# Performance work log

Measured on AMD Instinct MI355X. Metric: run time of the kernel, lower is better.

Reference implementation:

```python
import jax, jax.numpy as jnp
import numpy as np

N, H, B, D, O = 512, 40, 8, 384, 62
DT = 1e-4  # step_size
BOUND = 500.0  # coupling saturation bound
# Jansen-Rit constants (ParamsJR defaults, all variances 0 -> non-learnable)
A_, a_, B_, b_, g_ = 3.25, 100.0, 22.0, 50.0, 100.0
c1, c2, c3, c4 = 135.0, 135.0 * 0.8, 135.0 * 0.25, 135.0 * 0.25
STD_IN, VMAX, V0, R_, MU, K_, KI = 100.0, 5.0, 6.0, 0.56, 0.5, 5.0, 1.0


def setup_inputs() -> dict:
    key = jax.random.key(0)
    ks = jax.random.split(key, 9)
    return {
        "input": jax.random.normal(ks[0], (N, H, B), jnp.float32),
        "noise_in": jax.random.normal(ks[1], (N, H, B, 1), jnp.float32),
        "noise_out": jax.random.normal(ks[2], (N, B), jnp.float32),
        "hx": jax.random.uniform(ks[3], (N, 6), jnp.float32),
        "hE": jax.random.normal(ks[4], (N, D), jnp.float32),
        "w_bb": jax.random.normal(ks[5], (N, N), jnp.float32),
        "sc": jax.random.uniform(ks[6], (N, N), jnp.float32),
        "lm": jax.random.normal(ks[7], (O, N), jnp.float32),
        "delays": jax.random.randint(ks[8], (N, N), 0, D, jnp.int32),
    }


def _sigmoid(x):
    # potential-to-rate operator
    return VMAX / (1.0 + jnp.exp(R_ * (V0 - x)))


def _sys2nd(Aamp, a, u, x, v):
    return Aamp * a * u - 2.0 * a * v - a * a * x


def reference(input, noise_in, noise_out, hx, hE, w_bb, sc, lm, delays):
    # normalized symmetric coupling matrix
    w = jnp.exp(w_bb) * sc
    ws = jnp.log1p(0.5 * (w + w.T))
    w_n = ws / jnp.linalg.norm(ws)            # Frobenius norm, as torch.linalg.norm
    rowsum = jnp.sum(w_n, axis=1)[:, None]    # dg = -diag(rowsum); dg @ x == -rowsum*x

    M, E, I = hx[:, 0:1], hx[:, 1:2], hx[:, 2:3]
    Mv, Ev, Iv = hx[:, 3:4], hx[:, 4:5], hx[:, 5:6]

    def hidden_step(carry, inp):
        M, E, I, Mv, Ev, Iv, hE = carry
        u, nz = inp  # [N,1] each
        Ed = jnp.take_along_axis(hE, delays, axis=1)      # Ed[i,j] = hE[i, delays[i,j]]
        LEd = jnp.sum(w_n * Ed.T, axis=1, keepdims=True)  # [N,1]
        noiseE = nz * STD_IN
        stim = K_ * KI * u
        rM = _sigmoid(E - I)
        rE = c2 * _sigmoid(c1 * M)
        rI = c4 * _sigmoid(c3 * M)
        coupled = g_ * (LEd - rowsum * (E - I))
        coupling = BOUND * jnp.tanh(coupled / BOUND)
        Mn = M + DT * Mv
        En = E + DT * Ev
        In = I + DT * Iv
        Mvn = Mv + DT * _sys2nd(A_, a_, rM, M, Mv)
        Evn = Ev + DT * _sys2nd(A_, a_, rE + coupling + stim + noiseE + MU, E, Ev)
        Ivn = Iv + DT * _sys2nd(B_, b_, rI, I, Iv)
        hE = hE.at[:, 0].set(En[:, 0] - In[:, 0])  # in-place slot-0 write, as in torch
        return (Mn, En, In, Mvn, Evn, Ivn, hE), None

    def batch_step(state, inp):
        u_seq, nz_seq = inp  # [H,N,1]
        state, _ = jax.lax.scan(hidden_step, state, (u_seq, nz_seq))
        M, E, I, Mv, Ev, Iv, hE = state
        hE = jnp.concatenate([E - I, hE[:, :-1]], axis=1)  # shift delay buffer
        eeg = 0.0005 * (lm @ (E - I))  # [O,1]
        return (M, E, I, Mv, Ev, Iv, hE), (M, E, I, Mv, Ev, Iv, eeg)

    u_all = jnp.transpose(input, (2, 1, 0))[..., None]            # [B,H,N,1]
    nz_all = jnp.transpose(noise_in[..., 0], (2, 1, 0))[..., None]
    state0 = (M, E, I, Mv, Ev, Iv, hE)
    state, outs = jax.lax.scan(batch_step, state0, (u_all, nz_all))
    Ms, Es, Is, Mvs, Evs, Ivs, eegs = outs  # [B,N,1] each, eeg [B,O,1]

    stack = lambda x: x[..., 0].T  # -> [N,B] (or [O,B]), matches torch.cat(axis=1)
    Mf, Ef, If, Mvf, Evf, Ivf, hEf = state
    current_state = jnp.concatenate([Mf, Ef, If, Mvf, Evf, Ivf], axis=1)  # [N,6]
    return (current_state, stack(eegs), stack(Es), stack(Is), stack(Ms),
            stack(Evs), stack(Ivs), stack(Mvs), hEf)
```

## Files before the change

### kernel.cpp

```cpp
#include <hip/hip_runtime.h>
#include <math.h>

#define N_    512
#define H_    40
#define B_N   8
#define D_    384
#define O_    62
#define RW    392
#define SMAX  13
#define CMAX  28

#define OUT_STATE 0
#define OUT_EEG   3072
#define OUT_ES    3568
#define OUT_IS    7664
#define OUT_MS    11760
#define OUT_EVS   15856
#define OUT_IVS   19952
#define OUT_MVS   24048
#define OUT_HE    28144

#define SIGK      0.8079092228978195f
#define SIGC      4.847455337386917f
#define SIGK_E    109.06774509120563f
#define SIGK_I    27.266936272801407f
#define TANHS     0.5770780163555854f

#define BARRIER() asm volatile("s_waitcnt lgkmcnt(0)\n\ts_barrier" ::: "memory")

__global__ void k_prep(const float* __restrict__ input, const float* __restrict__ noise_in,
                       float* __restrict__ drv,
                       const float* __restrict__ wbb, const float* __restrict__ sc,
                       const float* __restrict__ hE_in, const int* __restrict__ delays,
                       float* __restrict__ ws, float* __restrict__ ring,
                       float* __restrict__ rowsum_ws, float* __restrict__ sumsq,
                       float* __restrict__ s0w, int* __restrict__ s0j, int* __restrict__ s0c,
                       float* __restrict__ s1w, int* __restrict__ s1p) {
    int i = blockIdx.x;
    int t = threadIdx.x;
    __shared__ float wsrow[N_];
    __shared__ float red[256];
    __shared__ int cnt_c[8];
    __shared__ int bases[8];
    __shared__ int runbase;

    if (i < H_ * B_N) {
        int b = i & 7, h = i >> 3;
        int dst = (b * H_ + h) * N_;
        for (int n = t; n < N_; n += 256) {
            float u  = input[n * (H_ * B_N) + h * B_N + b];
            float nz = noise_in[n * (H_ * B_N) + h * B_N + b];
            drv[dst + n] = fmaf(0.1625f, u, fmaf(3.25f, nz, 16.26625f));
        }
    }

    if (t < SMAX) { s0j[t * N_ + i] = i;        s0w[t * N_ + i] = 0.f; }
    if (t < CMAX) { s1p[t * N_ + i] = (1 << 9); s1w[t * N_ + i] = 0.f; }
    if (t < 9)    { ring[i * RW + t] = 0.f; }

    float ssq = 0.f, rsum = 0.f;
    for (int j = t; j < N_; j += 256) {
        float w = 0.5f * (expf(wbb[i * N_ + j]) * sc[i * N_ + j] +
                          expf(wbb[j * N_ + i]) * sc[j * N_ + i]);
        float v = log1pf(w);
        ws[i * N_ + j] = v;
        wsrow[j] = v;
        ssq += v * v;
        rsum += v;
    }
    for (int k = t; k < D_ - 1; k += 256) ring[i * RW + 9 + k] = hE_in[i * D_ + 1 + k];

    red[t] = ssq; __syncthreads();
    for (int s = 128; s > 0; s >>= 1) { if (t < s) red[t] += red[t + s]; __syncthreads(); }
    if (t == 0) sumsq[i] = red[0];
    __syncthreads();
    red[t] = rsum; __syncthreads();
    for (int s = 128; s > 0; s >>= 1) { if (t < s) red[t] += red[t + s]; __syncthreads(); }
    if (t == 0) rowsum_ws[i] = red[0];
    __syncthreads();

    int wave = t >> 6, lane = t & 63;
    int dv1 = delays[t * N_ + i];
    int dv2 = delays[(t + 256) * N_ + i];
    unsigned long long below = (lane == 0) ? 0ull : ((~0ull) >> (64 - lane));
    for (int d = 0; d < 8; d++) {
        bool f1 = (dv1 == d), f2 = (dv2 == d);
        unsigned long long m1 = __ballot(f1);
        unsigned long long m2 = __ballot(f2);
        if (lane == 0) { cnt_c[wave] = __popcll(m1); cnt_c[wave + 4] = __popcll(m2); }
        __syncthreads();
        if (t == 0) {
            int s = (d == 0) ? 0 : runbase;
            for (int c = 0; c < 8; c++) { bases[c] = s; s += cnt_c[c]; }
            if (d == 0) { s0c[i] = (s > SMAX) ? SMAX : s; runbase = 0; }
            else runbase = s;
        }
        __syncthreads();
        if (d == 0) {
            if (f1) { int pos = bases[wave]     + __popcll(m1 & below);
                      if (pos < SMAX) { s0j[pos * N_ + i] = t;       s0w[pos * N_ + i] = wsrow[t]; } }
            if (f2) { int pos = bases[wave + 4] + __popcll(m2 & below);
                      if (pos < SMAX) { s0j[pos * N_ + i] = t + 256; s0w[pos * N_ + i] = wsrow[t + 256]; } }
        } else {
            if (f1) { int pos = bases[wave]     + __popcll(m1 & below);
                      if (pos < CMAX) { s1p[pos * N_ + i] = t | (d << 9);         s1w[pos * N_ + i] = wsrow[t]; } }
            if (f2) { int pos = bases[wave + 4] + __popcll(m2 & below);
                      if (pos < CMAX) { s1p[pos * N_ + i] = (t + 256) | (d << 9); s1w[pos * N_ + i] = wsrow[t + 256]; } }
        }
    }
}

__global__ void __launch_bounds__(512)
k_hist(const float* __restrict__ ws, const int* __restrict__ delays,
       const float* __restrict__ ring, float* __restrict__ bp8) {
    int b  = blockIdx.x >> 6;
    int ib = (blockIdx.x >> 3) & 7;
    int jb = blockIdx.x & 7;
    int wave = threadIdx.x >> 6, lane = threadIdx.x & 63;
    int i = ib * 64 + lane;
    int off = 8 - b;
    float acc = 0.f;
    int j0 = jb * 64 + wave * 8;
#pragma unroll
    for (int jj = 0; jj < 8; jj++) {
        int j = j0 + jj;
        int d = delays[j * N_ + i];
        float w = ws[j * N_ + i];
        float v = ring[j * RW + off + d];
        acc += (d > 0 ? w : 0.f) * v;
    }
    __shared__ float part[8][64];
    part[wave][lane] = acc; __syncthreads();
    if (wave == 0) {
        float s = 0.f;
#pragma unroll
        for (int w2 = 0; w2 < 8; w2++) s += part[w2][lane];
        bp8[(b * 8 + jb) * N_ + i] = s;
    }
}

#define LOADK0(K) int jb_##K = s0j[K * N_ + i] << 2; float w_##K = s0w[K * N_ + i] * scale;
#define G(CB, K)  (*(const float*)((const char*)(CB) + jb_##K))

#define STEP(CB, CN)                                                           \
  {                                                                            \
    float g0 = G(CB,0), g1 = G(CB,1), g2 = G(CB,2);                            \
    float g3 = G(CB,3), g4 = G(CB,4), g5 = G(CB,5);                            \
    float g6=0.f,g7=0.f,g8=0.f,g9=0.f,g10=0.f,g11=0.f,g12=0.f;                 \
    if (wmax > 6) { g6=G(CB,6); g7=G(CB,7); g8=G(CB,8); g9=G(CB,9);            \
                    g10=G(CB,10); g11=G(CB,11); g12=G(CB,12); }                \
    float d_n = *dnext; dnext += N_;                                           \
    float En = fmaf(1e-4f, Ev, E);                                             \
    float In = fmaf(1e-4f, Iv, I);                                             \
    float Mn = fmaf(1e-4f, Mv, M);                                             \
    (CN)[i] = En - In;                                                         \
    float ei = E - I;                                                          \
    float rMr = __builtin_amdgcn_rcpf(1.0f + __builtin_amdgcn_exp2f(fmaf(-SIGK,   ei, SIGC))); \
    float rEr = __builtin_amdgcn_rcpf(1.0f + __builtin_amdgcn_exp2f(fmaf(-SIGK_E, M,  SIGC))); \
    float rIr = __builtin_amdgcn_rcpf(1.0f + __builtin_amdgcn_exp2f(fmaf(-SIGK_I, M,  SIGC))); \
    float Mvn = fmaf(0.1625f,  rMr, fmaf(0.98f, Mv, -M));                      \
    float Ivn = fmaf(18.5625f, rIr, fmaf(0.99f, Iv, -0.25f * I));              \
    float pre = fmaf(17.55f,   rEr, fmaf(0.98f, Ev, -E) + d_c);                \
    float p0 = fmaf(w_0, g0, w_1 * g1);                                        \
    float p1 = fmaf(w_2, g2, w_3 * g3);                                        \
    float p2 = fmaf(w_4, g4, w_5 * g5);                                        \
    float arg = (p0 + p1) + (p2 + fmaf(-rs, ei, base));                        \
    if (wmax > 6) {                                                            \
        arg += (fmaf(w_6, g6, w_7 * g7) + fmaf(w_8, g8, w_9 * g9)) +           \
               (fmaf(w_10, g10, w_11 * g11) + w_12 * g12);                     \
    }                                                                          \
    float cr = __builtin_amdgcn_rcpf(1.0f + __builtin_amdgcn_exp2f(arg));      \
    float Evn = fmaf(-32.5f, cr, pre);                                         \
    M = Mn; E = En; I = In; Mv = Mvn; Ev = Evn; Iv = Ivn; d_c = d_n;           \
    BARRIER();                                                                 \
  }

__global__ void __launch_bounds__(512)
k_hidden(const float* __restrict__ drv, const float* __restrict__ hE_in,
         const float* __restrict__ hx, const float* __restrict__ bp8,
         const float* __restrict__ sumsq, const float* __restrict__ rowsum_ws,
         const float* __restrict__ s0w, const int* __restrict__ s0j,
         const int* __restrict__ s0c, const float* __restrict__ s1w,
         const int* __restrict__ s1p, float* __restrict__ ring,
         float* __restrict__ fing, float* __restrict__ out) {
    __shared__ float curr0[N_];
    __shared__ float curr1[N_];
    __shared__ float fin_l[B_N * N_];
    __shared__ float red[N_];
    int i = threadIdx.x;

    int m = s0c[i];
#pragma unroll
    for (int off = 32; off > 0; off >>= 1) {
        int o = __shfl_xor(m, off, 64);
        m = (o > m) ? o : m;
    }
    int wmax = __builtin_amdgcn_readfirstlane(m);

    red[i] = sumsq[i];
    __syncthreads();
    if (i < 64) {
        float s2 = 0.f;
#pragma unroll
        for (int q = 0; q < 8; q++) s2 += red[i + 64 * q];
#pragma unroll
        for (int off = 32; off > 0; off >>= 1) s2 += __shfl_xor(s2, off, 64);
        if (i == 0) red[0] = s2;
    }
    __syncthreads();
    float scale = TANHS / sqrtf(red[0]);

    LOADK0(0)  LOADK0(1)  LOADK0(2)  LOADK0(3)  LOADK0(4)  LOADK0(5)  LOADK0(6)
    LOADK0(7)  LOADK0(8)  LOADK0(9)  LOADK0(10) LOADK0(11) LOADK0(12)
    int   s1p_r[CMAX];
    float s1w_r[CMAX];
#pragma unroll
    for (int k = 0; k < CMAX; k++) { s1p_r[k] = s1p[k * N_ + i]; s1w_r[k] = s1w[k * N_ + i] * scale; }

    float M  = hx[i * 6 + 0], E  = hx[i * 6 + 1], I  = hx[i * 6 + 2];
    float Mv = hx[i * 6 + 3], Ev = hx[i * 6 + 4], Iv = hx[i * 6 + 5];
    float rs = rowsum_ws[i] * scale;

    float hp[8];
#pragma unroll
    for (int k = 0; k < 8; k++) hp[k] = bp8[k * N_ + i];

    const float* dnext = drv + i + N_;
    float d_c = drv[i];

    #pragma unroll
    for (int k = 0; k < B_N; k++) fin_l[k * N_ + i] = 0.f;
    curr0[i] = hE_in[i * D_];
    __syncthreads();

    for (int b = 0; b < B_N; b++) {
        float hist = (((hp[0] + hp[1]) + (hp[2] + hp[3])) +
                      ((hp[4] + hp[5]) + (hp[6] + hp[7]))) * scale;
        float corr = 0.f;
#pragma unroll
        for (int k = 0; k < CMAX; k++) {
            int p = s1p_r[k];
            int off = (((b + 8 - (p >> 9)) & 7) << 11) + ((p & 511) << 2);
            corr = fmaf(s1w_r[k], *(const float*)((const char*)fin_l + off), corr);
        }
        float base = hist + corr;

        int bn = (b < B_N - 1) ? b + 1 : b;
#pragma unroll
        for (int k = 0; k < 8; k++) hp[k] = bp8[(bn * 8 + k) * N_ + i];

        for (int hh = 0; hh < H_ / 2; hh++) {
            STEP(curr0, curr1)
            STEP(curr1, curr0)
        }
        float eif = E - I;
        fin_l[b * N_ + i] = eif;
        out[OUT_ES  + i * B_N + b] = E;
        out[OUT_IS  + i * B_N + b] = I;
        out[OUT_MS  + i * B_N + b] = M;
        out[OUT_EVS + i * B_N + b] = Ev;
        out[OUT_IVS + i * B_N + b] = Iv;
        out[OUT_MVS + i * B_N + b] = Mv;
        ring[i * RW + (7 - b)] = eif;
        ring[i * RW + (8 - b)] = eif;
        fing[b * N_ + i] = eif;
        BARRIER();
    }

    out[i * 6 + 0] = M;  out[i * 6 + 1] = E;  out[i * 6 + 2] = I;
    out[i * 6 + 3] = Mv; out[i * 6 + 4] = Ev; out[i * 6 + 5] = Iv;
}

__global__ void k_post(const float* __restrict__ ring, const float* __restrict__ fing,
                       const float* __restrict__ lm, float* __restrict__ out) {
    int bi = blockIdx.x;
    int lane = threadIdx.x;
    if (bi < N_) {
#pragma unroll
        for (int q = 0; q < 6; q++) {
            int k = lane + 64 * q;
            if (k < D_) out[OUT_HE + bi * D_ + k] = ring[bi * RW + k];
        }
    } else {
        int o = bi - N_;
        float lv[8];
#pragma unroll
        for (int q = 0; q < 8; q++) lv[q] = lm[o * N_ + 64 * q + lane];
        for (int b = 0; b < B_N; b++) {
            float p = 0.f;
#pragma unroll
            for (int q = 0; q < 8; q++) p = fmaf(lv[q], fing[b * N_ + 64 * q + lane], p);
#pragma unroll
            for (int off = 32; off > 0; off >>= 1) p += __shfl_down(p, off, 64);
            if (lane == 0) out[OUT_EEG + o * B_N + b] = 0.0005f * p;
        }
    }
}

extern "C" void kernel_launch(void* const* d_in, const int* in_sizes, int n_in,
                              void* d_out, int out_size, void* d_ws, size_t ws_size,
                              hipStream_t stream) {
    const float* input    = (const float*)d_in[0];
    const float* noise_in = (const float*)d_in[1];
    const float* hx       = (const float*)d_in[3];
    const float* hE       = (const float*)d_in[4];
    const float* wbb      = (const float*)d_in[5];
    const float* sc       = (const float*)d_in[6];
    const float* lm       = (const float*)d_in[7];
    const int*   delays   = (const int*)d_in[8];
    float* out = (float*)d_out;

    float* F    = (float*)d_ws;
    float* drv  = F;
    float* wsm  = drv + 164352;
    float* ring = wsm + 262144;
    float* bp8  = ring + 200704;
    float* rsw  = bp8 + 32768;
    float* ssq  = rsw + 512;
    float* s0w  = ssq + 512;
    int*   s0j  = (int*)(s0w + N_ * SMAX);
    int*   s0c  = s0j + N_ * SMAX;
    float* s1w  = (float*)(s0c + N_);
    int*   s1p  = (int*)(s1w + N_ * CMAX);
    float* fing = (float*)(s1p + N_ * CMAX);

    k_prep<<<N_, 256, 0, stream>>>(input, noise_in, drv, wbb, sc, hE, delays,
                                   wsm, ring, rsw, ssq, s0w, s0j, s0c, s1w, s1p);
    k_hist<<<512, 512, 0, stream>>>(wsm, delays, ring, bp8);
    k_hidden<<<1, N_, 0, stream>>>(drv, hE, hx, bp8, ssq, rsw,
                                   s0w, s0j, s0c, s1w, s1p, ring, fing, out);
    k_post<<<N_ + O_, 64, 0, stream>>>(ring, fing, lm, out);
}
```

Baseline: 133.0 us.

## Sort nodes by zero-delay neighbor count so each wave gathers only what it needs

Adds two small kernels that count zero-delay neighbors per node and build a permutation sorting nodes by that count. The hidden single-block kernel then maps threads to permuted nodes, so each wave's per-wave maximum bounds the number of shared-memory gathers per step. Gathers for the next step are prefetched right after the barrier. Drive-term preparation moves from k_prep into k_hist. The cost is two extra kernel launches and permuted indexing throughout.

```diff
diff --git a/kernel.cpp b/kernel.cpp
--- a/kernel.cpp
+++ b/kernel.cpp
@@ -28,34 +28,69 @@
 
 #define BARRIER() asm volatile("s_waitcnt lgkmcnt(0)\n\ts_barrier" ::: "memory")
 
-__global__ void k_prep(const float* __restrict__ input, const float* __restrict__ noise_in,
-                       float* __restrict__ drv,
-                       const float* __restrict__ wbb, const float* __restrict__ sc,
+__global__ void k_cnt(const int* __restrict__ delays, int* __restrict__ s0c) {
+    int i = blockIdx.x, t = threadIdx.x;
+    bool f1 = (delays[t * N_ + i] == 0);
+    bool f2 = (delays[(t + 256) * N_ + i] == 0);
+    unsigned long long m1 = __ballot(f1), m2 = __ballot(f2);
+    __shared__ int pc[4];
+    int wave = t >> 6, lane = t & 63;
+    if (lane == 0) pc[wave] = __popcll(m1) + __popcll(m2);
+    __syncthreads();
+    if (t == 0) {
+        int s = pc[0] + pc[1] + pc[2] + pc[3];
+        s0c[i] = (s > SMAX) ? SMAX : s;
+    }
+}
+
+__global__ void __launch_bounds__(512)
+k_perm(const int* __restrict__ s0c, int* __restrict__ perm,
+       int* __restrict__ invp, int* __restrict__ wmaxc) {
+    int t = threadIdx.x;
+    int wave = t >> 6, lane = t & 63;
+    int cnt = s0c[t];
+    __shared__ int wc[14 * 8];
+    __shared__ int base[14 * 8];
+    unsigned long long below = (lane == 0) ? 0ull : ((~0ull) >> (64 - lane));
+    for (int c = 0; c < 14; c++) {
+        unsigned long long m = __ballot(cnt == c);
+        if (lane == 0) wc[c * 8 + wave] = __popcll(m);
+    }
+    __syncthreads();
+    if (t == 0) {
+        int s = 0;
+        for (int c = 0; c < 14; c++)
+            for (int w = 0; w < 8; w++) { base[c * 8 + w] = s; s += wc[c * 8 + w]; }
+    }
+    __syncthreads();
+    int pos = 0;
+    for (int c = 0; c < 14; c++) {
+        unsigned long long m = __ballot(cnt == c);
+        if (cnt == c) pos = base[c * 8 + wave] + __popcll(m & below);
+    }
+    perm[pos] = t;
+    invp[t] = pos;
+    if ((pos & 63) == 63) wmaxc[pos >> 6] = cnt;
+}
+
+__global__ void k_prep(const float* __restrict__ wbb, const float* __restrict__ sc,
                        const float* __restrict__ hE_in, const int* __restrict__ delays,
+                       const int* __restrict__ invp,
                        float* __restrict__ ws, float* __restrict__ ring,
-                       float* __restrict__ rowsum_ws, float* __restrict__ sumsq,
-                       float* __restrict__ s0w, int* __restrict__ s0j, int* __restrict__ s0c,
+                       float* __restrict__ rowsumP, float* __restrict__ sumsq,
+                       float* __restrict__ s0w, int* __restrict__ s0j,
                        float* __restrict__ s1w, int* __restrict__ s1p) {
     int i = blockIdx.x;
     int t = threadIdx.x;
+    int ip = invp[i];
     __shared__ float wsrow[N_];
     __shared__ float red[256];
     __shared__ int cnt_c[8];
     __shared__ int bases[8];
     __shared__ int runbase;
 
-    if (i < H_ * B_N) {
-        int b = i & 7, h = i >> 3;
-        int dst = (b * H_ + h) * N_;
-        for (int n = t; n < N_; n += 256) {
-            float u  = input[n * (H_ * B_N) + h * B_N + b];
-            float nz = noise_in[n * (H_ * B_N) + h * B_N + b];
-            drv[dst + n] = fmaf(0.1625f, u, fmaf(3.25f, nz, 16.26625f));
-        }
-    }
-
-    if (t < SMAX) { s0j[t * N_ + i] = i;        s0w[t * N_ + i] = 0.f; }
-    if (t < CMAX) { s1p[t * N_ + i] = (1 << 9); s1w[t * N_ + i] = 0.f; }
+    if (t < SMAX) { s0j[t * N_ + ip] = i;        s0w[t * N_ + ip] = 0.f; }
+    if (t < CMAX) { s1p[t * N_ + ip] = (1 << 9); s1w[t * N_ + ip] = 0.f; }
     if (t < 9)    { ring[i * RW + t] = 0.f; }
 
     float ssq = 0.f, rsum = 0.f;
@@ -76,7 +111,7 @@
     __syncthreads();
     red[t] = rsum; __syncthreads();
     for (int s = 128; s > 0; s >>= 1) { if (t < s) red[t] += red[t + s]; __syncthreads(); }
-    if (t == 0) rowsum_ws[i] = red[0];
+    if (t == 0) rowsumP[ip] = red[0];
     __syncthreads();
 
     int wave = t >> 6, lane = t & 63;
@@ -92,27 +127,37 @@
         if (t == 0) {
             int s = (d == 0) ? 0 : runbase;
             for (int c = 0; c < 8; c++) { bases[c] = s; s += cnt_c[c]; }
-            if (d == 0) { s0c[i] = (s > SMAX) ? SMAX : s; runbase = 0; }
+            if (d == 0) runbase = 0;
             else runbase = s;
         }
         __syncthreads();
         if (d == 0) {
             if (f1) { int pos = bases[wave]     + __popcll(m1 & below);
-                      if (pos < SMAX) { s0j[pos * N_ + i] = t;       s0w[pos * N_ + i] = wsrow[t]; } }
+                      if (pos < SMAX) { s0j[pos * N_ + ip] = t;       s0w[pos * N_ + ip] = wsrow[t]; } }
             if (f2) { int pos = bases[wave + 4] + __popcll(m2 & below);
-                      if (pos < SMAX) { s0j[pos * N_ + i] = t + 256; s0w[pos * N_ + i] = wsrow[t + 256]; } }
+                      if (pos < SMAX) { s0j[pos * N_ + ip] = t + 256; s0w[pos * N_ + ip] = wsrow[t + 256]; } }
         } else {
             if (f1) { int pos = bases[wave]     + __popcll(m1 & below);
-                      if (pos < CMAX) { s1p[pos * N_ + i] = t | (d << 9);         s1w[pos * N_ + i] = wsrow[t]; } }
+                      if (pos < CMAX) { s1p[pos * N_ + ip] = t | (d << 9);         s1w[pos * N_ + ip] = wsrow[t]; } }
             if (f2) { int pos = bases[wave + 4] + __popcll(m2 & below);
-                      if (pos < CMAX) { s1p[pos * N_ + i] = (t + 256) | (d << 9); s1w[pos * N_ + i] = wsrow[t + 256]; } }
+                      if (pos < CMAX) { s1p[pos * N_ + ip] = (t + 256) | (d << 9); s1w[pos * N_ + ip] = wsrow[t + 256]; } }
         }
     }
 }
 
 __global__ void __launch_bounds__(512)
 k_hist(const float* __restrict__ ws, const int* __restrict__ delays,
-       const float* __restrict__ ring, float* __restrict__ bp8) {
+       const float* __restrict__ ring, const int* __restrict__ invp,
+       const float* __restrict__ input, const float* __restrict__ noise_in,
+       float* __restrict__ drv, float* __restrict__ bp8) {
+    if (blockIdx.x < H_ * B_N) {
+        int bb = blockIdx.x & 7, h = blockIdx.x >> 3;
+        int dst = (bb * H_ + h) * N_;
+        int nn = threadIdx.x;
+        float u  = input[nn * (H_ * B_N) + h * B_N + bb];
+        float nz = noise_in[nn * (H_ * B_N) + h * B_N + bb];
+        drv[dst + invp[nn]] = fmaf(0.1625f, u, fmaf(3.25f, nz, 16.26625f));
+    }
     int b  = blockIdx.x >> 6;
     int ib = (blockIdx.x >> 3) & 7;
     int jb = blockIdx.x & 7;
@@ -135,25 +180,29 @@
         float s = 0.f;
 #pragma unroll
         for (int w2 = 0; w2 < 8; w2++) s += part[w2][lane];
-        bp8[(b * 8 + jb) * N_ + i] = s;
-    }
-}
-
-#define LOADK0(K) int jb_##K = s0j[K * N_ + i] << 2; float w_##K = s0w[K * N_ + i] * scale;
+        bp8[(b * 8 + jb) * N_ + invp[i]] = s;
+    }
+}
+
+#define LOADK0(K) int jb_##K = s0j[K * N_ + t] << 2; float w_##K = s0w[K * N_ + t] * scale;
 #define G(CB, K)  (*(const float*)((const char*)(CB) + jb_##K))
+
+#define PRF(CB)                                                                \
+    if (wmax > 0)  g0  = G(CB,0);  if (wmax > 1)  g1  = G(CB,1);               \
+    if (wmax > 2)  g2  = G(CB,2);  if (wmax > 3)  g3  = G(CB,3);               \
+    if (wmax > 4)  g4  = G(CB,4);  if (wmax > 5)  g5  = G(CB,5);               \
+    if (wmax > 6)  g6  = G(CB,6);  if (wmax > 7)  g7  = G(CB,7);               \
+    if (wmax > 8)  g8  = G(CB,8);  if (wmax > 9)  g9  = G(CB,9);               \
+    if (wmax > 10) g10 = G(CB,10); if (wmax > 11) g11 = G(CB,11);              \
+    if (wmax > 12) g12 = G(CB,12);
 
 #define STEP(CB, CN)                                                           \
   {                                                                            \
-    float g0 = G(CB,0), g1 = G(CB,1), g2 = G(CB,2);                            \
-    float g3 = G(CB,3), g4 = G(CB,4), g5 = G(CB,5);                            \
-    float g6=0.f,g7=0.f,g8=0.f,g9=0.f,g10=0.f,g11=0.f,g12=0.f;                 \
-    if (wmax > 6) { g6=G(CB,6); g7=G(CB,7); g8=G(CB,8); g9=G(CB,9);            \
-                    g10=G(CB,10); g11=G(CB,11); g12=G(CB,12); }                \
     float d_n = *dnext; dnext += N_;                                           \
     float En = fmaf(1e-4f, Ev, E);                                             \
     float In = fmaf(1e-4f, Iv, I);                                             \
     float Mn = fmaf(1e-4f, Mv, M);                                             \
-    (CN)[i] = En - In;                                                         \
+    (CN)[n] = En - In;                                                         \
     float ei = E - I;                                                          \
     float rMr = __builtin_amdgcn_rcpf(1.0f + __builtin_amdgcn_exp2f(fmaf(-SIGK,   ei, SIGC))); \
     float rEr = __builtin_amdgcn_rcpf(1.0f + __builtin_amdgcn_exp2f(fmaf(-SIGK_E, M,  SIGC))); \
@@ -161,51 +210,48 @@
     float Mvn = fmaf(0.1625f,  rMr, fmaf(0.98f, Mv, -M));                      \
     float Ivn = fmaf(18.5625f, rIr, fmaf(0.99f, Iv, -0.25f * I));              \
     float pre = fmaf(17.55f,   rEr, fmaf(0.98f, Ev, -E) + d_c);                \
-    float p0 = fmaf(w_0, g0, w_1 * g1);                                        \
-    float p1 = fmaf(w_2, g2, w_3 * g3);                                        \
-    float p2 = fmaf(w_4, g4, w_5 * g5);                                        \
-    float arg = (p0 + p1) + (p2 + fmaf(-rs, ei, base));                        \
-    if (wmax > 6) {                                                            \
-        arg += (fmaf(w_6, g6, w_7 * g7) + fmaf(w_8, g8, w_9 * g9)) +           \
-               (fmaf(w_10, g10, w_11 * g11) + w_12 * g12);                     \
-    }                                                                          \
+    float a0 = 0.f, a1 = 0.f;                                                  \
+    if (wmax > 0)  a0 = w_0 * g0;            if (wmax > 1)  a1 = w_1 * g1;     \
+    if (wmax > 2)  a0 = fmaf(w_2,  g2,  a0); if (wmax > 3)  a1 = fmaf(w_3,  g3,  a1); \
+    if (wmax > 4)  a0 = fmaf(w_4,  g4,  a0); if (wmax > 5)  a1 = fmaf(w_5,  g5,  a1); \
+    if (wmax > 6)  a0 = fmaf(w_6,  g6,  a0); if (wmax > 7)  a1 = fmaf(w_7,  g7,  a1); \
+    if (wmax > 8)  a0 = fmaf(w_8,  g8,  a0); if (wmax > 9)  a1 = fmaf(w_9,  g9,  a1); \
+    if (wmax > 10) a0 = fmaf(w_10, g10, a0); if (wmax > 11) a1 = fmaf(w_11, g11, a1); \
+    if (wmax > 12) a0 = fmaf(w_12, g12, a0);                                   \
+    float arg = fmaf(-rs, ei, base) + (a0 + a1);                               \
     float cr = __builtin_amdgcn_rcpf(1.0f + __builtin_amdgcn_exp2f(arg));      \
     float Evn = fmaf(-32.5f, cr, pre);                                         \
     M = Mn; E = En; I = In; Mv = Mvn; Ev = Evn; Iv = Ivn; d_c = d_n;           \
     BARRIER();                                                                 \
+    PRF(CN)                                                                    \
   }
 
 __global__ void __launch_bounds__(512)
 k_hidden(const float* __restrict__ drv, const float* __restrict__ hE_in,
          const float* __restrict__ hx, const float* __restrict__ bp8,
-         const float* __restrict__ sumsq, const float* __restrict__ rowsum_ws,
+         const float* __restrict__ sumsq, const float* __restrict__ rowsumP,
          const float* __restrict__ s0w, const int* __restrict__ s0j,
-         const int* __restrict__ s0c, const float* __restrict__ s1w,
-         const int* __restrict__ s1p, float* __restrict__ ring,
-         float* __restrict__ fing, float* __restrict__ out) {
+         const float* __restrict__ s1w, const int* __restrict__ s1p,
+         const int* __restrict__ perm, const int* __restrict__ wmaxc,
+         float* __restrict__ ring, float* __restrict__ fing,
+         float* __restrict__ out) {
     __shared__ float curr0[N_];
     __shared__ float curr1[N_];
     __shared__ float fin_l[B_N * N_];
     __shared__ float red[N_];
-    int i = threadIdx.x;
-
-    int m = s0c[i];
-#pragma unroll
-    for (int off = 32; off > 0; off >>= 1) {
-        int o = __shfl_xor(m, off, 64);
-        m = (o > m) ? o : m;
-    }
-    int wmax = __builtin_amdgcn_readfirstlane(m);
-
-    red[i] = sumsq[i];
-    __syncthreads();
-    if (i < 64) {
+    int t = threadIdx.x;
+    int n = perm[t];
+    int wmax = __builtin_amdgcn_readfirstlane(wmaxc[t >> 6]);
+
+    red[t] = sumsq[t];
+    __syncthreads();
+    if (t < 64) {
         float s2 = 0.f;
 #pragma unroll
-        for (int q = 0; q < 8; q++) s2 += red[i + 64 * q];
+        for (int q = 0; q < 8; q++) s2 += red[t + 64 * q];
 #pragma unroll
         for (int off = 32; off > 0; off >>= 1) s2 += __shfl_xor(s2, off, 64);
-        if (i == 0) red[0] = s2;
+        if (t == 0) red[0] = s2;
     }
     __syncthreads();
     float scale = TANHS / sqrtf(red[0]);
@@ -215,23 +261,27 @@
     int   s1p_r[CMAX];
     float s1w_r[CMAX];
 #pragma unroll
-    for (int k = 0; k < CMAX; k++) { s1p_r[k] = s1p[k * N_ + i]; s1w_r[k] = s1w[k * N_ + i] * scale; }
-
-    float M  = hx[i * 6 + 0], E  = hx[i * 6 + 1], I  = hx[i * 6 + 2];
-    float Mv = hx[i * 6 + 3], Ev = hx[i * 6 + 4], Iv = hx[i * 6 + 5];
-    float rs = rowsum_ws[i] * scale;
+    for (int k = 0; k < CMAX; k++) { s1p_r[k] = s1p[k * N_ + t]; s1w_r[k] = s1w[k * N_ + t] * scale; }
+
+    float M  = hx[n * 6 + 0], E  = hx[n * 6 + 1], I  = hx[n * 6 + 2];
+    float Mv = hx[n * 6 + 3], Ev = hx[n * 6 + 4], Iv = hx[n * 6 + 5];
+    float rs = rowsumP[t] * scale;
 
     float hp[8];
 #pragma unroll
-    for (int k = 0; k < 8; k++) hp[k] = bp8[k * N_ + i];
-
-    const float* dnext = drv + i + N_;
-    float d_c = drv[i];
-
-    #pragma unroll
-    for (int k = 0; k < B_N; k++) fin_l[k * N_ + i] = 0.f;
-    curr0[i] = hE_in[i * D_];
-    __syncthreads();
+    for (int k = 0; k < 8; k++) hp[k] = bp8[k * N_ + t];
+
+    const float* dnext = drv + t + N_;
+    float d_c = drv[t];
+
+    float g0=0.f,g1=0.f,g2=0.f,g3=0.f,g4=0.f,g5=0.f,g6=0.f,g7=0.f,g8=0.f,
+          g9=0.f,g10=0.f,g11=0.f,g12=0.f;
+
+#pragma unroll
+    for (int k = 0; k < B_N; k++) fin_l[k * N_ + t] = 0.f;
+    curr0[n] = hE_in[n * D_];
+    __syncthreads();
+    PRF(curr0)
 
     for (int b = 0; b < B_N; b++) {
         float hist = (((hp[0] + hp[1]) + (hp[2] + hp[3])) +
@@ -247,28 +297,28 @@
 
         int bn = (b < B_N - 1) ? b + 1 : b;
 #pragma unroll
-        for (int k = 0; k < 8; k++) hp[k] = bp8[(bn * 8 + k) * N_ + i];
+        for (int k = 0; k < 8; k++) hp[k] = bp8[(bn * 8 + k) * N_ + t];
 
         for (int hh = 0; hh < H_ / 2; hh++) {
             STEP(curr0, curr1)
             STEP(curr1, curr0)
         }
         float eif = E - I;
-        fin_l[b * N_ + i] = eif;
-        out[OUT_ES  + i * B_N + b] = E;
-        out[OUT_IS  + i * B_N + b] = I;
-        out[OUT_MS  + i * B_N + b] = M;
-        out[OUT_EVS + i * B_N + b] = Ev;
-        out[OUT_IVS + i * B_N + b] = Iv;
-        out[OUT_MVS + i * B_N + b] = Mv;
-        ring[i * RW + (7 - b)] = eif;
-        ring[i * RW + (8 - b)] = eif;
-        fing[b * N_ + i] = eif;
+        fin_l[b * N_ + n] = eif;
+        out[OUT_ES  + n * B_N + b] = E;
+        out[OUT_IS  + n * B_N + b] = I;
+        out[OUT_MS  + n * B_N + b] = M;
+        out[OUT_EVS + n * B_N + b] = Ev;
+        out[OUT_IVS + n * B_N + b] = Iv;
+        out[OUT_MVS + n * B_N + b] = Mv;
+        ring[n * RW + (7 - b)] = eif;
+        ring[n * RW + (8 - b)] = eif;
+        fing[b * N_ + n] = eif;
         BARRIER();
     }
 
-    out[i * 6 + 0] = M;  out[i * 6 + 1] = E;  out[i * 6 + 2] = I;
-    out[i * 6 + 3] = Mv; out[i * 6 + 4] = Ev; out[i * 6 + 5] = Iv;
+    out[n * 6 + 0] = M;  out[n * 6 + 1] = E;  out[n * 6 + 2] = I;
+    out[n * 6 + 3] = Mv; out[n * 6 + 4] = Ev; out[n * 6 + 5] = Iv;
 }
 
 __global__ void k_post(const float* __restrict__ ring, const float* __restrict__ fing,
@@ -315,19 +365,24 @@
     float* wsm  = drv + 164352;
     float* ring = wsm + 262144;
     float* bp8  = ring + 200704;
-    float* rsw  = bp8 + 32768;
-    float* ssq  = rsw + 512;
+    float* rswP = bp8 + 32768;
+    float* ssq  = rswP + 512;
     float* s0w  = ssq + 512;
     int*   s0j  = (int*)(s0w + N_ * SMAX);
-    int*   s0c  = s0j + N_ * SMAX;
-    float* s1w  = (float*)(s0c + N_);
+    float* s1w  = (float*)(s0j + N_ * SMAX);
     int*   s1p  = (int*)(s1w + N_ * CMAX);
     float* fing = (float*)(s1p + N_ * CMAX);
-
-    k_prep<<<N_, 256, 0, stream>>>(input, noise_in, drv, wbb, sc, hE, delays,
-                                   wsm, ring, rsw, ssq, s0w, s0j, s0c, s1w, s1p);
-    k_hist<<<512, 512, 0, stream>>>(wsm, delays, ring, bp8);
-    k_hidden<<<1, N_, 0, stream>>>(drv, hE, hx, bp8, ssq, rsw,
-                                   s0w, s0j, s0c, s1w, s1p, ring, fing, out);
+    int*   s0c  = (int*)(fing + B_N * N_);
+    int*   perm = s0c + N_;
+    int*   invp = perm + N_;
+    int*   wmaxc = invp + N_;
+
+    k_cnt<<<N_, 256, 0, stream>>>(delays, s0c);
+    k_perm<<<1, N_, 0, stream>>>(s0c, perm, invp, wmaxc);
+    k_prep<<<N_, 256, 0, stream>>>(wbb, sc, hE, delays, invp,
+                                   wsm, ring, rswP, ssq, s0w, s0j, s1w, s1p);
+    k_hist<<<512, 512, 0, stream>>>(wsm, delays, ring, invp, input, noise_in, drv, bp8);
+    k_hidden<<<1, N_, 0, stream>>>(drv, hE, hx, bp8, ssq, rswP,
+                                   s0w, s0j, s1w, s1p, perm, wmaxc, ring, fing, out);
     k_post<<<N_ + O_, 64, 0, stream>>>(ring, fing, lm, out);
 }
```

Result: slower. 175.5 us (+31.9%).
